# Performance work log

Measured on AMD Instinct MI355X. Metric: run time of the kernel, lower is better.

## Reference

```python
import jax, jax.numpy as jnp
import numpy as np

N, M = 32768, 12          # atoms, neighbors
ORIG, NBR, AF, HF = 92, 41, 64, 128
N_CONV = 3
ATOMS_PER = 32            # atoms per crystal
B = N // ATOMS_PER        # number of crystals
EPS = 1e-5                # BatchNorm eps


def softplus(x):
    return jnp.logaddexp(x, 0.0)


def setup_inputs() -> dict:
    key = jax.random.key(0)
    ks = jax.random.split(key, 24)
    s = 0.05
    return {
        "atom_fea": jax.random.normal(ks[0], (N, ORIG), jnp.float32),
        "nbr_fea": jax.random.normal(ks[1], (N, M, NBR), jnp.float32),
        "nbr_fea_idx": jax.random.randint(ks[2], (N, M), 0, N),
        "crystal_id": jnp.arange(N, dtype=jnp.int32) // ATOMS_PER,
        # embedding: Linear(ORIG -> AF)
        "emb_W": jax.random.normal(ks[3], (ORIG, AF), jnp.float32) * s,
        "emb_b": jnp.zeros((AF,), jnp.float32),
        # per-conv-layer params, stacked over N_CONV
        "conv_W": jax.random.normal(ks[4], (N_CONV, 2 * AF + NBR, 2 * AF), jnp.float32) * s,
        "conv_b": jnp.zeros((N_CONV, 2 * AF), jnp.float32),
        "bn1_g": jnp.ones((N_CONV, 2 * AF), jnp.float32),
        "bn1_b": jnp.zeros((N_CONV, 2 * AF), jnp.float32),
        "bn2_g": jnp.ones((N_CONV, AF), jnp.float32),
        "bn2_b": jnp.zeros((N_CONV, AF), jnp.float32),
        # head: conv_to_fc (AF->HF), fcs[0] (HF->HF), fc_out (HF->1)
        "fc1_W": jax.random.normal(ks[5], (AF, HF), jnp.float32) * s,
        "fc1_b": jnp.zeros((HF,), jnp.float32),
        "fc2_W": jax.random.normal(ks[6], (HF, HF), jnp.float32) * s,
        "fc2_b": jnp.zeros((HF,), jnp.float32),
        "out_W": jax.random.normal(ks[7], (HF, 1), jnp.float32) * s,
        "out_b": jnp.zeros((1,), jnp.float32),
    }


def _batchnorm(x, g, b):
    # training-mode BN over the batch (row) axis, biased variance like torch
    mu = x.mean(axis=0)
    var = x.var(axis=0)
    return (x - mu) * jax.lax.rsqrt(var + EPS) * g + b


def reference(atom_fea, nbr_fea, nbr_fea_idx, crystal_id,
              emb_W, emb_b, conv_W, conv_b, bn1_g, bn1_b, bn2_g, bn2_b,
              fc1_W, fc1_b, fc2_W, fc2_b, out_W, out_b):
    x = atom_fea @ emb_W + emb_b                              # (N, AF)
    for l in range(N_CONV):
        nbr_atom = x[nbr_fea_idx]                             # gather (N, M, AF)
        self_fea = jnp.broadcast_to(x[:, None, :], (N, M, AF))
        tot = jnp.concatenate([self_fea, nbr_atom, nbr_fea], axis=2)  # (N,M,2AF+NBR)
        g = tot @ conv_W[l] + conv_b[l]                       # (N, M, 2AF)
        g = _batchnorm(g.reshape(N * M, 2 * AF), bn1_g[l], bn1_b[l]).reshape(N, M, 2 * AF)
        nbr_filter = jax.nn.sigmoid(g[..., :AF])
        nbr_core = softplus(g[..., AF:])
        summed = jnp.sum(nbr_filter * nbr_core, axis=1)       # (N, AF)
        summed = _batchnorm(summed, bn2_g[l], bn2_b[l])
        x = softplus(x + summed)
    # mean pooling per crystal (equal-size crystals of ATOMS_PER atoms)
    pool = jax.ops.segment_sum(x, crystal_id, num_segments=B) / ATOMS_PER  # (B, AF)
    # seq2: softplus -> conv_to_fc -> dropout(p=0) -> softplus -> Linear -> softplus -> dropout(p=0)
    h = softplus(pool)
    h = softplus(h @ fc1_W + fc1_b)
    h = softplus(h @ fc2_W + fc2_b)
    return h @ out_W + out_b                                  # (B, 1)
```

## Files before the change

kernel.cpp:

```cpp
#include <hip/hip_runtime.h>
#include <cmath>

#define DEV __device__ __forceinline__

constexpr int NA    = 32768;
constexpr int M     = 12;
constexpr int ORIG  = 92;
constexpr int NBR   = 41;
constexpr int AF    = 64;
constexpr int C2    = 128;
constexpr int HF    = 128;
constexpr int NCONV = 3;
constexpr int NM    = NA * M;
constexpr int BB    = 1024;
constexpr int TA    = 4;
constexpr int RT    = TA * M;
constexpr int NTILES = NA / TA;
constexpr int GRID_CONV = 4096;
constexpr int TSTRIDE = GRID_CONV / 2;
constexpr int GRID_APPLY = 2048;
constexpr int WLD2  = 68;
constexpr int ALD   = 44;

DEV float fsig(float x) { return __builtin_amdgcn_rcpf(1.f + __expf(-x)); }
DEV float fsp (float x) { return fmaxf(x, 0.f) + __logf(1.f + __expf(-fabsf(x))); }

DEV void fma4(float4& a, float s, const float4 w) {
    a.x = fmaf(s, w.x, a.x); a.y = fmaf(s, w.y, a.y);
    a.z = fmaf(s, w.z, a.z); a.w = fmaf(s, w.w, a.w);
}
DEV void fma2(float2& a, float s, const float2 w) {
    a.x = fmaf(s, w.x, a.x); a.y = fmaf(s, w.y, a.y);
}
DEV float comp4(const float4 v, int i) { return i == 0 ? v.x : i == 1 ? v.y : i == 2 ? v.z : v.w; }
DEV void add2(float2& a, const float2 b) { a.x += b.x; a.y += b.y; }
DEV void sqa2(float2& a, const float2 b) { a.x = fmaf(b.x, b.x, a.x); a.y = fmaf(b.y, b.y, a.y); }
DEV float2 shxor2(const float2 v, int m) {
    float2 r; r.x = __shfl_xor(v.x, m, 64); r.y = __shfl_xor(v.y, m, 64); return r;
}
DEV void bfly2(float2& v) {
    float2 t = shxor2(v, 16); add2(v, t);
    t = shxor2(v, 32); add2(v, t);
}
DEV unsigned bf16pair(float a, float b) {
    unsigned ua = __float_as_uint(a), ub = __float_as_uint(b);
    ua += 0x7fffu + ((ua >> 16) & 1u);
    ub += 0x7fffu + ((ub >> 16) & 1u);
    return (ua >> 16) | (ub & 0xffff0000u);
}
DEV float2 up2(unsigned u) {
    float2 r;
    r.x = __uint_as_float(u << 16);
    r.y = __uint_as_float(u & 0xffff0000u);
    return r;
}

template<bool FIRST>
__global__ __launch_bounds__(256, 4)
void spx_kernel(const float* __restrict__ xin,
                const float* __restrict__ summed,
                const float* __restrict__ ss2,
                const float* __restrict__ atom_fea,
                const float* __restrict__ embW,
                const float* __restrict__ embb,
                const float* __restrict__ W,
                const float* __restrict__ bias,
                float* __restrict__ xout,
                float* __restrict__ S,
                unsigned* __restrict__ Pb)
{
    __shared__ float xs[16][AF];
    __shared__ float af[FIRST ? 16 * ORIG : 4];

    const int a0 = blockIdx.x * 16, tid = threadIdx.x;

    if (FIRST) {
        for (int i = tid; i < 16 * ORIG; i += 256) af[i] = atom_fea[(size_t)a0 * ORIG + i];
        __syncthreads();
        const int row = tid >> 4, c4 = (tid & 15) * 4;
        float4 acc = *(const float4*)(embb + c4);
        #pragma unroll 4
        for (int k = 0; k < ORIG; ++k)
            fma4(acc, af[row * ORIG + k], *(const float4*)(embW + k * AF + c4));
        *(float4*)&xs[row][c4] = acc;
        *(float4*)(xout + (size_t)(a0 + row) * AF + c4) = acc;
    } else {
        const int row = tid >> 4, c4 = (tid & 15) * 4;
        const size_t o = (size_t)(a0 + row) * AF + c4;
        const float4 xi = *(const float4*)(xin + o);
        const float4 sm = *(const float4*)(summed + o);
        const float4 sc = *(const float4*)(ss2 + c4);
        const float4 sh = *(const float4*)(ss2 + AF + c4);
        float4 ov;
        ov.x = fsp(xi.x + fmaf(sm.x, sc.x, sh.x));
        ov.y = fsp(xi.y + fmaf(sm.y, sc.y, sh.y));
        ov.z = fsp(xi.z + fmaf(sm.z, sc.z, sh.z));
        ov.w = fsp(xi.w + fmaf(sm.w, sc.w, sh.w));
        *(float4*)&xs[row][c4] = ov;
        *(float4*)(xout + o) = ov;
    }
    __syncthreads();

    const int cid = tid & 31, rid = tid >> 5;
    const int c0 = cid * 8, r0 = rid * 2;
    const bool isS = (c0 < 128);
    const int cc = c0 & 127;
    const float* Wb = W + (isS ? 0 : AF * C2) + cc;
    float4 a00, a01, a10, a11;
    if (isS) { a00 = *(const float4*)(bias + cc); a01 = *(const float4*)(bias + cc + 4); }
    else     { a00 = {0,0,0,0}; a01 = {0,0,0,0}; }
    a10 = a00; a11 = a01;
    for (int k = 0; k < AF; ++k) {
        const float4 w0 = *(const float4*)(Wb + k * C2);
        const float4 w1 = *(const float4*)(Wb + k * C2 + 4);
        const float x0 = xs[r0][k], x1 = xs[r0 + 1][k];
        fma4(a00, x0, w0); fma4(a01, x0, w1);
        fma4(a10, x1, w0); fma4(a11, x1, w1);
    }
    if (isS) {
        *(float4*)(S + (size_t)(a0 + r0) * C2 + cc)     = a00;
        *(float4*)(S + (size_t)(a0 + r0) * C2 + cc + 4) = a01;
        *(float4*)(S + (size_t)(a0 + r0 + 1) * C2 + cc)     = a10;
        *(float4*)(S + (size_t)(a0 + r0 + 1) * C2 + cc + 4) = a11;
    } else {
        uint4 u0, u1;
        u0.x = bf16pair(a00.x, a00.y); u0.y = bf16pair(a00.z, a00.w);
        u0.z = bf16pair(a01.x, a01.y); u0.w = bf16pair(a01.z, a01.w);
        u1.x = bf16pair(a10.x, a10.y); u1.y = bf16pair(a10.z, a10.w);
        u1.z = bf16pair(a11.x, a11.y); u1.w = bf16pair(a11.z, a11.w);
        *(uint4*)(Pb + (size_t)(a0 + r0) * 64 + cc / 2)     = u0;
        *(uint4*)(Pb + (size_t)(a0 + r0 + 1) * 64 + cc / 2) = u1;
    }
}

__global__ __launch_bounds__(256, 4)
void conv8_kernel(const float* __restrict__ nbr_fea,
                  const int* __restrict__ idx,
                  const float* __restrict__ W2,
                  const float* __restrict__ S,
                  const unsigned* __restrict__ Pb,
                  float* __restrict__ P1s, float* __restrict__ P1q,
                  unsigned* __restrict__ gout)
{
    __shared__ float W2h[NBR * WLD2];
    __shared__ float sA[RT * ALD];

    const int tid  = threadIdx.x;
    const int cid  = tid & 15;
    const int rid  = tid >> 4;
    const int ch   = blockIdx.x & 1;
    const int c2   = cid * 2;
    const int gf   = ch * 32 + c2;
    const int gc   = 64 + gf;
    const int r0   = rid * 3;
    const int atom = tid >> 6;

    const int q0 = blockIdx.x >> 1;

    int j0, j1, j2;
    float2 svf, svc;
    float st[8];
    {
        const int n0 = q0 * TA;
        const int ib = n0 * M + r0;
        j0 = idx[ib]; j1 = idx[ib + 1]; j2 = idx[ib + 2];
        svf = *(const float2*)(S + (size_t)(n0 + atom) * C2 + gf);
        svc = *(const float2*)(S + (size_t)(n0 + atom) * C2 + gc);
        const float* src = nbr_fea + (size_t)n0 * M * NBR;
        #pragma unroll
        for (int i = 0; i < 8; ++i)
            if (tid + 256 * i < RT * NBR) st[i] = src[tid + 256 * i];
    }

    for (int i = tid; i < NBR * 16; i += 256) {
        const int k = i >> 4, q = i & 15;
        const int srcc = (q < 8) ? (ch * 32 + q * 4) : (64 + ch * 32 + (q - 8) * 4);
        *(float4*)&W2h[k * WLD2 + q * 4] = *(const float4*)(W2 + k * C2 + srcc);
    }

    int soff[8];
    #pragma unroll
    for (int i = 0; i < 8; ++i) {
        const int e = tid + 256 * i;
        if (e < RT * NBR) {
            const int r = (int)(((unsigned)e * 102301u) >> 22);
            soff[i] = r * ALD + (e - r * NBR);
        } else soff[i] = -1;
    }

    float2 sum_f = {0,0}, sum_c = {0,0}, sq_f = {0,0}, sq_c = {0,0};

    for (int it = 0; it < 4; ++it) {
        const int t  = q0 + it * TSTRIDE;
        const int n0 = t * TA;

        const unsigned u0f = Pb[(size_t)j0 * 64 + ch * 16 + cid];
        const unsigned u0c = Pb[(size_t)j0 * 64 + 32 + ch * 16 + cid];
        const unsigned u1f = Pb[(size_t)j1 * 64 + ch * 16 + cid];
        const unsigned u1c = Pb[(size_t)j1 * 64 + 32 + ch * 16 + cid];
        const unsigned u2f = Pb[(size_t)j2 * 64 + ch * 16 + cid];
        const unsigned u2c = Pb[(size_t)j2 * 64 + 32 + ch * 16 + cid];

        const float2 cf = svf, cc = svc;

        __syncthreads();
        #pragma unroll
        for (int i = 0; i < 8; ++i) if (soff[i] >= 0) sA[soff[i]] = st[i];
        __syncthreads();

        if (it < 3) {
            const int nn0 = (t + TSTRIDE) * TA;
            const int ib = nn0 * M + r0;
            j0 = idx[ib]; j1 = idx[ib + 1]; j2 = idx[ib + 2];
            svf = *(const float2*)(S + (size_t)(nn0 + atom) * C2 + gf);
            svc = *(const float2*)(S + (size_t)(nn0 + atom) * C2 + gc);
            const float* src = nbr_fea + (size_t)nn0 * M * NBR;
            #pragma unroll
            for (int i = 0; i < 8; ++i)
                if (tid + 256 * i < RT * NBR) st[i] = src[tid + 256 * i];
        }

        float2 ef0 = {0,0}, ec0 = {0,0}, ef1 = {0,0}, ec1 = {0,0}, ef2 = {0,0}, ec2 = {0,0};
        const float4* A0 = (const float4*)(sA + (r0 + 0) * ALD);
        const float4* A1 = (const float4*)(sA + (r0 + 1) * ALD);
        const float4* A2 = (const float4*)(sA + (r0 + 2) * ALD);
        #pragma unroll 2
        for (int k4 = 0; k4 < 10; ++k4) {
            const float4 a0 = A0[k4], a1 = A1[k4], a2 = A2[k4];
            #pragma unroll
            for (int kk = 0; kk < 4; ++kk) {
                const int k = 4 * k4 + kk;
                const float2 wf = *(const float2*)(W2h + k * WLD2 + c2);
                const float2 wc = *(const float2*)(W2h + k * WLD2 + 32 + c2);
                fma2(ef0, comp4(a0, kk), wf); fma2(ec0, comp4(a0, kk), wc);
                fma2(ef1, comp4(a1, kk), wf); fma2(ec1, comp4(a1, kk), wc);
                fma2(ef2, comp4(a2, kk), wf); fma2(ec2, comp4(a2, kk), wc);
            }
        }
        {
            const float2 wf = *(const float2*)(W2h + 40 * WLD2 + c2);
            const float2 wc = *(const float2*)(W2h + 40 * WLD2 + 32 + c2);
            const float a0s = sA[(r0 + 0) * ALD + 40];
            const float a1s = sA[(r0 + 1) * ALD + 40];
            const float a2s = sA[(r0 + 2) * ALD + 40];
            fma2(ef0, a0s, wf); fma2(ec0, a0s, wc);
            fma2(ef1, a1s, wf); fma2(ec1, a1s, wc);
            fma2(ef2, a2s, wf); fma2(ec2, a2s, wc);
        }

        add2(ef0, cf); add2(ef0, up2(u0f));
        add2(ec0, cc); add2(ec0, up2(u0c));
        add2(ef1, cf); add2(ef1, up2(u1f));
        add2(ec1, cc); add2(ec1, up2(u1c));
        add2(ef2, cf); add2(ef2, up2(u2f));
        add2(ec2, cc); add2(ec2, up2(u2c));

        {
            const size_t row0 = (size_t)(n0 * M + r0) * 64 + ch * 16 + cid;
            gout[row0]       = bf16pair(ef0.x, ef0.y);
            gout[row0 + 32]  = bf16pair(ec0.x, ec0.y);
            gout[row0 + 64]  = bf16pair(ef1.x, ef1.y);
            gout[row0 + 96]  = bf16pair(ec1.x, ec1.y);
            gout[row0 + 128] = bf16pair(ef2.x, ef2.y);
            gout[row0 + 160] = bf16pair(ec2.x, ec2.y);
        }

        add2(sum_f, ef0); add2(sum_f, ef1); add2(sum_f, ef2);
        add2(sum_c, ec0); add2(sum_c, ec1); add2(sum_c, ec2);
        sqa2(sq_f, ef0);  sqa2(sq_f, ef1);  sqa2(sq_f, ef2);
        sqa2(sq_c, ec0);  sqa2(sq_c, ec1);  sqa2(sq_c, ec2);
    }

    bfly2(sum_f); bfly2(sum_c); bfly2(sq_f); bfly2(sq_c);
    __syncthreads();
    if ((tid & 48) == 0) {
        *(float2*)&sA[atom * 64 + c2]            = sum_f;
        *(float2*)&sA[atom * 64 + 32 + c2]       = sum_c;
        *(float2*)&sA[256 + atom * 64 + c2]      = sq_f;
        *(float2*)&sA[256 + atom * 64 + 32 + c2] = sq_c;
    }
    __syncthreads();
    if (tid < 64) {
        P1s[(size_t)blockIdx.x * 64 + tid] = sA[tid] + sA[64 + tid] + sA[128 + tid] + sA[192 + tid];
        P1q[(size_t)blockIdx.x * 64 + tid] = sA[256 + tid] + sA[256 + 64 + tid]
                                           + sA[256 + 128 + tid] + sA[256 + 192 + tid];
    }
}

__global__ __launch_bounds__(256)
void apply_g_kernel(const unsigned* __restrict__ g,
                    const float* __restrict__ ss1,
                    float* __restrict__ summed,
                    float* __restrict__ P2s, float* __restrict__ P2q)
{
    const int tid = threadIdx.x;
    const int al  = tid >> 5;
    const int c2  = tid & 31;
    const int cA  = 2 * c2;
    const float2 scf = *(const float2*)(ss1 + cA);
    const float2 scc = *(const float2*)(ss1 + 64 + cA);
    const float2 shf = *(const float2*)(ss1 + C2 + cA);
    const float2 shc = *(const float2*)(ss1 + C2 + 64 + cA);
    float2 ts = {0.f, 0.f}, tq = {0.f, 0.f};

    for (int grp = blockIdx.x; grp < NA / 8; grp += gridDim.x) {
        const int a = grp * 8 + al;
        const unsigned* gr = g + (size_t)a * M * 64 + c2;
        float2 acc = {0.f, 0.f};
        #pragma unroll
        for (int m = 0; m < M; ++m) {
            const unsigned uf = gr[m * 64];
            const unsigned us = gr[m * 64 + 32];
            const float2 f = up2(uf);
            const float2 s = up2(us);
            acc.x = fmaf(fsig(fmaf(f.x, scf.x, shf.x)), fsp(fmaf(s.x, scc.x, shc.x)), acc.x);
            acc.y = fmaf(fsig(fmaf(f.y, scf.y, shf.y)), fsp(fmaf(s.y, scc.y, shc.y)), acc.y);
        }
        *(float2*)(summed + (size_t)a * AF + cA) = acc;
        ts.x += acc.x; ts.y += acc.y;
        tq.x = fmaf(acc.x, acc.x, tq.x); tq.y = fmaf(acc.y, acc.y, tq.y);
    }

    __shared__ float2 rs[8][32], rq[8][32];
    rs[al][c2] = ts; rq[al][c2] = tq;
    __syncthreads();
    if (tid < 32) {
        float2 s = rs[0][tid], q = rq[0][tid];
        #pragma unroll
        for (int a = 1; a < 8; ++a) {
            s.x += rs[a][tid].x; s.y += rs[a][tid].y;
            q.x += rq[a][tid].x; q.y += rq[a][tid].y;
        }
        *(float2*)(P2s + (size_t)blockIdx.x * AF + 2 * tid) = s;
        *(float2*)(P2q + (size_t)blockIdx.x * AF + 2 * tid) = q;
    }
}

__global__ __launch_bounds__(256)
void bn_finalize_half(const float* __restrict__ Ps, const float* __restrict__ Pq,
                      int rowlen, float invn,
                      const float* __restrict__ gamma, const float* __restrict__ beta,
                      float* __restrict__ ss, int Ctot)
{
    __shared__ float sd[256];
    const int c = blockIdx.x, tid = threadIdx.x;
    const int ch = (c >> 5) & 1;
    const int lc = (c & 31) + ((c >= 64) ? 32 : 0);
    float s = 0.f;
    for (int i = tid; i < TSTRIDE; i += 256) s += Ps[(size_t)(ch + 2 * i) * rowlen + lc];
    sd[tid] = s; __syncthreads();
    for (int st = 128; st > 0; st >>= 1) { if (tid < st) sd[tid] += sd[tid + st]; __syncthreads(); }
    const float total = sd[0];
    __syncthreads();
    float q = 0.f;
    for (int i = tid; i < TSTRIDE; i += 256) q += Pq[(size_t)(ch + 2 * i) * rowlen + lc];
    sd[tid] = q; __syncthreads();
    for (int st = 128; st > 0; st >>= 1) { if (tid < st) sd[tid] += sd[tid + st]; __syncthreads(); }
    if (tid == 0) {
        const float mean = total * invn;
        const float var  = sd[0] * invn - mean * mean;
        const float scl  = gamma[c] * rsqrtf(var + 1e-5f);
        ss[c]        = scl;
        ss[Ctot + c] = beta[c] - mean * scl;
    }
}

__global__ __launch_bounds__(256)
void bn_finalize_plain(const float* __restrict__ Ps, const float* __restrict__ Pq,
                       int npart, int C, float invn,
                       const float* __restrict__ gamma, const float* __restrict__ beta,
                       float* __restrict__ ss)
{
    __shared__ float sd[256];
    const int c = blockIdx.x, tid = threadIdx.x;
    float s = 0.f;
    for (int j = tid; j < npart; j += 256) s += Ps[(size_t)j * C + c];
    sd[tid] = s; __syncthreads();
    for (int st = 128; st > 0; st >>= 1) { if (tid < st) sd[tid] += sd[tid + st]; __syncthreads(); }
    const float total = sd[0];
    __syncthreads();
    float q = 0.f;
    for (int j = tid; j < npart; j += 256) q += Pq[(size_t)j * C + c];
    sd[tid] = q; __syncthreads();
    for (int st = 128; st > 0; st >>= 1) { if (tid < st) sd[tid] += sd[tid + st]; __syncthreads(); }
    if (tid == 0) {
        const float mean = total * invn;
        const float var  = sd[0] * invn - mean * mean;
        const float scl  = gamma[c] * rsqrtf(var + 1e-5f);
        ss[c]     = scl;
        ss[C + c] = beta[c] - mean * scl;
    }
}

__global__ __launch_bounds__(128)
void head_kernel(const float* __restrict__ x,
                 const float* __restrict__ summed,
                 const float* __restrict__ ss2,
                 const float* __restrict__ fc1W, const float* __restrict__ fc1b,
                 const float* __restrict__ fc2W, const float* __restrict__ fc2b,
                 const float* __restrict__ outW, const float* __restrict__ outb,
                 float* __restrict__ out)
{
    __shared__ float l0[AF], l1[HF], rr[2], hs[2][AF];
    const int b = blockIdx.x, tid = threadIdx.x;
    const int col = tid & 63, half = tid >> 6;
    {
        const float sc = ss2[col], sh = ss2[AF + col];
        float s = 0.f;
        #pragma unroll 4
        for (int a = half * 16; a < half * 16 + 16; ++a) {
            const size_t o = (size_t)(b * 32 + a) * AF + col;
            s += fsp(x[o] + fmaf(summed[o], sc, sh));
        }
        hs[half][col] = s;
    }
    __syncthreads();
    if (tid < AF) l0[tid] = fsp((hs[0][tid] + hs[1][tid]) * (1.f / 32.f));
    __syncthreads();
    float acc = fc1b[tid];
    #pragma unroll 4
    for (int k = 0; k < AF; ++k) acc = fmaf(l0[k], fc1W[k * HF + tid], acc);
    l1[tid] = fsp(acc);
    __syncthreads();
    acc = fc2b[tid];
    #pragma unroll 4
    for (int k = 0; k < HF; ++k) acc = fmaf(l1[k], fc2W[k * HF + tid], acc);
    float v = fsp(acc) * outW[tid];
    #pragma unroll
    for (int off = 32; off > 0; off >>= 1) v += __shfl_down(v, off, 64);
    if ((tid & 63) == 0) rr[tid >> 6] = v;
    __syncthreads();
    if (tid == 0) out[b] = rr[0] + rr[1] + outb[0];
}

extern "C" void kernel_launch(void* const* d_in, const int* in_sizes, int n_in,
                              void* d_out, int out_size, void* d_ws, size_t ws_size,
                              hipStream_t stream)
{
    const float* atom_fea = (const float*)d_in[0];
    const float* nbr_fea  = (const float*)d_in[1];
    const int*   nbr_idx  = (const int*)d_in[2];
    const float* emb_W  = (const float*)d_in[4];
    const float* emb_b  = (const float*)d_in[5];
    const float* conv_W = (const float*)d_in[6];
    const float* conv_b = (const float*)d_in[7];
    const float* bn1_g  = (const float*)d_in[8];
    const float* bn1_b  = (const float*)d_in[9];
    const float* bn2_g  = (const float*)d_in[10];
    const float* bn2_b  = (const float*)d_in[11];
    const float* fc1W   = (const float*)d_in[12];
    const float* fc1b   = (const float*)d_in[13];
    const float* fc2W   = (const float*)d_in[14];
    const float* fc2b   = (const float*)d_in[15];
    const float* outW   = (const float*)d_in[16];
    const float* outb   = (const float*)d_in[17];
    float* out = (float*)d_out;
    float* ws  = (float*)d_ws;

    float*    x_a    = ws;
    float*    x_b    = x_a + (size_t)NA * AF;
    float*    Sbuf   = x_b + (size_t)NA * AF;
    unsigned* Pb     = (unsigned*)(Sbuf + (size_t)NA * C2);
    float*    summed = (float*)(Pb + (size_t)NA * 64);
    float*    P1s    = summed + (size_t)NA * AF;
    float*    P1q    = P1s + (size_t)GRID_CONV * 64;
    float*    P2s    = P1q + (size_t)GRID_CONV * 64;
    float*    P2q    = P2s + (size_t)GRID_APPLY * AF;
    float*    ss1    = P2q + (size_t)GRID_APPLY * AF;
    float*    ss2    = ss1 + 2 * C2;
    unsigned* gbuf   = (unsigned*)(ss2 + 2 * AF);

    float* xcur = x_a;
    spx_kernel<true><<<NA / 16, 256, 0, stream>>>(nullptr, nullptr, nullptr,
                                                  atom_fea, emb_W, emb_b,
                                                  conv_W, conv_b, xcur, Sbuf, Pb);
    for (int l = 0; l < NCONV; ++l) {
        const float* W2 = conv_W + (size_t)l * (C2 + NBR) * C2 + (size_t)C2 * C2;
        conv8_kernel<<<GRID_CONV, 256, 0, stream>>>(nbr_fea, nbr_idx, W2,
                                                    Sbuf, Pb, P1s, P1q, gbuf);
        bn_finalize_half<<<C2, 256, 0, stream>>>(P1s, P1q, 64, 1.f / (float)NM,
                                                 bn1_g + l * C2, bn1_b + l * C2, ss1, C2);
        apply_g_kernel<<<GRID_APPLY, 256, 0, stream>>>(gbuf, ss1, summed, P2s, P2q);
        bn_finalize_plain<<<AF, 256, 0, stream>>>(P2s, P2q, GRID_APPLY, AF, 1.f / (float)NA,
                                                  bn2_g + l * AF, bn2_b + l * AF, ss2);
        if (l < NCONV - 1) {
            float* xnext = (xcur == x_a) ? x_b : x_a;
            spx_kernel<false><<<NA / 16, 256, 0, stream>>>(xcur, summed, ss2,
                                                           nullptr, nullptr, nullptr,
                                                           conv_W + (size_t)(l + 1) * (C2 + NBR) * C2,
                                                           conv_b + (size_t)(l + 1) * C2,
                                                           xnext, Sbuf, Pb);
            xcur = xnext;
        }
    }
    head_kernel<<<BB, 128, 0, stream>>>(xcur, summed, ss2,
                                        fc1W, fc1b, fc2W, fc2b, outW, outb, out);
}
```

Baseline: 641.7 us.

## Have each conv block cover all 128 channels with six rows per thread

```diff
diff --git a/kernel.cpp b/kernel.cpp
--- a/kernel.cpp
+++ b/kernel.cpp
@@ -16,10 +16,9 @@
 constexpr int TA    = 4;
 constexpr int RT    = TA * M;
 constexpr int NTILES = NA / TA;
-constexpr int GRID_CONV = 4096;
-constexpr int TSTRIDE = GRID_CONV / 2;
+constexpr int GRID_CONV = 2048;
 constexpr int GRID_APPLY = 2048;
-constexpr int WLD2  = 68;
+constexpr int WLD   = 132;
 constexpr int ALD   = 44;
 
 DEV float fsig(float x) { return __builtin_amdgcn_rcpf(1.f + __expf(-x)); }
@@ -37,10 +36,6 @@
 DEV void sqa2(float2& a, const float2 b) { a.x = fmaf(b.x, b.x, a.x); a.y = fmaf(b.y, b.y, a.y); }
 DEV float2 shxor2(const float2 v, int m) {
     float2 r; r.x = __shfl_xor(v.x, m, 64); r.y = __shfl_xor(v.y, m, 64); return r;
-}
-DEV void bfly2(float2& v) {
-    float2 t = shxor2(v, 16); add2(v, t);
-    t = shxor2(v, 32); add2(v, t);
 }
 DEV unsigned bf16pair(float a, float b) {
     unsigned ua = __float_as_uint(a), ub = __float_as_uint(b);
@@ -142,148 +137,162 @@
                   float* __restrict__ P1s, float* __restrict__ P1q,
                   unsigned* __restrict__ gout)
 {
-    __shared__ float W2h[NBR * WLD2];
+    __shared__ float W2h[NBR * WLD];
     __shared__ float sA[RT * ALD];
 
     const int tid  = threadIdx.x;
-    const int cid  = tid & 15;
-    const int rid  = tid >> 4;
-    const int ch   = blockIdx.x & 1;
+    const int cid  = tid & 31;
+    const int rid  = tid >> 5;
     const int c2   = cid * 2;
-    const int gf   = ch * 32 + c2;
-    const int gc   = 64 + gf;
-    const int r0   = rid * 3;
-    const int atom = tid >> 6;
-
-    const int q0 = blockIdx.x >> 1;
-
-    int j0, j1, j2;
+    const int r0   = rid * 6;
+    const int atom = rid >> 1;
+
+    const int q0 = blockIdx.x;
+
+    int j[6];
     float2 svf, svc;
     float st[8];
     {
         const int n0 = q0 * TA;
         const int ib = n0 * M + r0;
-        j0 = idx[ib]; j1 = idx[ib + 1]; j2 = idx[ib + 2];
-        svf = *(const float2*)(S + (size_t)(n0 + atom) * C2 + gf);
-        svc = *(const float2*)(S + (size_t)(n0 + atom) * C2 + gc);
+        #pragma unroll
+        for (int e = 0; e < 6; ++e) j[e] = idx[ib + e];
+        svf = *(const float2*)(S + (size_t)(n0 + atom) * C2 + c2);
+        svc = *(const float2*)(S + (size_t)(n0 + atom) * C2 + 64 + c2);
         const float* src = nbr_fea + (size_t)n0 * M * NBR;
         #pragma unroll
         for (int i = 0; i < 8; ++i)
-            if (tid + 256 * i < RT * NBR) st[i] = src[tid + 256 * i];
-    }
-
-    for (int i = tid; i < NBR * 16; i += 256) {
-        const int k = i >> 4, q = i & 15;
-        const int srcc = (q < 8) ? (ch * 32 + q * 4) : (64 + ch * 32 + (q - 8) * 4);
-        *(float4*)&W2h[k * WLD2 + q * 4] = *(const float4*)(W2 + k * C2 + srcc);
-    }
-
-    int soff[8];
-    #pragma unroll
-    for (int i = 0; i < 8; ++i) {
-        const int e = tid + 256 * i;
-        if (e < RT * NBR) {
-            const int r = (int)(((unsigned)e * 102301u) >> 22);
-            soff[i] = r * ALD + (e - r * NBR);
-        } else soff[i] = -1;
+            if (i < 7 || tid + 256 * i < RT * NBR) st[i] = src[tid + 256 * i];
+    }
+
+    for (int i = tid; i < NBR * 32; i += 256) {
+        const int k = i >> 5, q = i & 31;
+        *(float4*)&W2h[k * WLD + q * 4] = *(const float4*)(W2 + k * C2 + q * 4);
     }
 
     float2 sum_f = {0,0}, sum_c = {0,0}, sq_f = {0,0}, sq_c = {0,0};
 
     for (int it = 0; it < 4; ++it) {
-        const int t  = q0 + it * TSTRIDE;
+        const int t  = q0 + it * GRID_CONV;
         const int n0 = t * TA;
 
-        const unsigned u0f = Pb[(size_t)j0 * 64 + ch * 16 + cid];
-        const unsigned u0c = Pb[(size_t)j0 * 64 + 32 + ch * 16 + cid];
-        const unsigned u1f = Pb[(size_t)j1 * 64 + ch * 16 + cid];
-        const unsigned u1c = Pb[(size_t)j1 * 64 + 32 + ch * 16 + cid];
-        const unsigned u2f = Pb[(size_t)j2 * 64 + ch * 16 + cid];
-        const unsigned u2c = Pb[(size_t)j2 * 64 + 32 + ch * 16 + cid];
-
+        unsigned uf[6], uc[6];
+        #pragma unroll
+        for (int e = 0; e < 6; ++e) {
+            uf[e] = Pb[(size_t)j[e] * 64 + cid];
+            uc[e] = Pb[(size_t)j[e] * 64 + 32 + cid];
+        }
         const float2 cf = svf, cc = svc;
 
         __syncthreads();
         #pragma unroll
-        for (int i = 0; i < 8; ++i) if (soff[i] >= 0) sA[soff[i]] = st[i];
+        for (int i = 0; i < 8; ++i) {
+            const int e = tid + 256 * i;
+            if (i < 7 || e < RT * NBR) {
+                const int r = (int)(((unsigned)e * 102301u) >> 22);
+                sA[r * ALD + (e - r * NBR)] = st[i];
+            }
+        }
         __syncthreads();
 
         if (it < 3) {
-            const int nn0 = (t + TSTRIDE) * TA;
+            const int nn0 = (t + GRID_CONV) * TA;
             const int ib = nn0 * M + r0;
-            j0 = idx[ib]; j1 = idx[ib + 1]; j2 = idx[ib + 2];
-            svf = *(const float2*)(S + (size_t)(nn0 + atom) * C2 + gf);
-            svc = *(const float2*)(S + (size_t)(nn0 + atom) * C2 + gc);
+            #pragma unroll
+            for (int e = 0; e < 6; ++e) j[e] = idx[ib + e];
+            svf = *(const float2*)(S + (size_t)(nn0 + atom) * C2 + c2);
+            svc = *(const float2*)(S + (size_t)(nn0 + atom) * C2 + 64 + c2);
             const float* src = nbr_fea + (size_t)nn0 * M * NBR;
             #pragma unroll
             for (int i = 0; i < 8; ++i)
-                if (tid + 256 * i < RT * NBR) st[i] = src[tid + 256 * i];
-        }
-
-        float2 ef0 = {0,0}, ec0 = {0,0}, ef1 = {0,0}, ec1 = {0,0}, ef2 = {0,0}, ec2 = {0,0};
-        const float4* A0 = (const float4*)(sA + (r0 + 0) * ALD);
-        const float4* A1 = (const float4*)(sA + (r0 + 1) * ALD);
-        const float4* A2 = (const float4*)(sA + (r0 + 2) * ALD);
+                if (i < 7 || tid + 256 * i < RT * NBR) st[i] = src[tid + 256 * i];
+        }
+
+        float2 ef0 = {0,0}, ef1 = {0,0}, ef2 = {0,0}, ef3 = {0,0}, ef4 = {0,0}, ef5 = {0,0};
+        float2 ec0 = {0,0}, ec1 = {0,0}, ec2 = {0,0}, ec3 = {0,0}, ec4 = {0,0}, ec5 = {0,0};
+        const float* Ab = sA + r0 * ALD;
         #pragma unroll 2
         for (int k4 = 0; k4 < 10; ++k4) {
-            const float4 a0 = A0[k4], a1 = A1[k4], a2 = A2[k4];
+            const float4 a0 = *(const float4*)(Ab + 0 * ALD + k4 * 4);
+            const float4 a1 = *(const float4*)(Ab + 1 * ALD + k4 * 4);
+            const float4 a2 = *(const float4*)(Ab + 2 * ALD + k4 * 4);
+            const float4 a3 = *(const float4*)(Ab + 3 * ALD + k4 * 4);
+            const float4 a4 = *(const float4*)(Ab + 4 * ALD + k4 * 4);
+            const float4 a5 = *(const float4*)(Ab + 5 * ALD + k4 * 4);
             #pragma unroll
             for (int kk = 0; kk < 4; ++kk) {
                 const int k = 4 * k4 + kk;
-                const float2 wf = *(const float2*)(W2h + k * WLD2 + c2);
-                const float2 wc = *(const float2*)(W2h + k * WLD2 + 32 + c2);
+                const float2 wf = *(const float2*)(W2h + k * WLD + c2);
+                const float2 wc = *(const float2*)(W2h + k * WLD + 64 + c2);
                 fma2(ef0, comp4(a0, kk), wf); fma2(ec0, comp4(a0, kk), wc);
                 fma2(ef1, comp4(a1, kk), wf); fma2(ec1, comp4(a1, kk), wc);
                 fma2(ef2, comp4(a2, kk), wf); fma2(ec2, comp4(a2, kk), wc);
+                fma2(ef3, comp4(a3, kk), wf); fma2(ec3, comp4(a3, kk), wc);
+                fma2(ef4, comp4(a4, kk), wf); fma2(ec4, comp4(a4, kk), wc);
+                fma2(ef5, comp4(a5, kk), wf); fma2(ec5, comp4(a5, kk), wc);
             }
         }
         {
-            const float2 wf = *(const float2*)(W2h + 40 * WLD2 + c2);
-            const float2 wc = *(const float2*)(W2h + 40 * WLD2 + 32 + c2);
-            const float a0s = sA[(r0 + 0) * ALD + 40];
-            const float a1s = sA[(r0 + 1) * ALD + 40];
-            const float a2s = sA[(r0 + 2) * ALD + 40];
-            fma2(ef0, a0s, wf); fma2(ec0, a0s, wc);
-            fma2(ef1, a1s, wf); fma2(ec1, a1s, wc);
-            fma2(ef2, a2s, wf); fma2(ec2, a2s, wc);
-        }
-
-        add2(ef0, cf); add2(ef0, up2(u0f));
-        add2(ec0, cc); add2(ec0, up2(u0c));
-        add2(ef1, cf); add2(ef1, up2(u1f));
-        add2(ec1, cc); add2(ec1, up2(u1c));
-        add2(ef2, cf); add2(ef2, up2(u2f));
-        add2(ec2, cc); add2(ec2, up2(u2c));
-
+            const float2 wf = *(const float2*)(W2h + 40 * WLD + c2);
+            const float2 wc = *(const float2*)(W2h + 40 * WLD + 64 + c2);
+            const float b0 = Ab[0 * ALD + 40], b1 = Ab[1 * ALD + 40], b2 = Ab[2 * ALD + 40];
+            const float b3 = Ab[3 * ALD + 40], b4 = Ab[4 * ALD + 40], b5 = Ab[5 * ALD + 40];
+            fma2(ef0, b0, wf); fma2(ec0, b0, wc);
+            fma2(ef1, b1, wf); fma2(ec1, b1, wc);
+            fma2(ef2, b2, wf); fma2(ec2, b2, wc);
+            fma2(ef3, b3, wf); fma2(ec3, b3, wc);
+            fma2(ef4, b4, wf); fma2(ec4, b4, wc);
+            fma2(ef5, b5, wf); fma2(ec5, b5, wc);
+        }
+
+        const size_t row0 = (size_t)(n0 * M + r0) * 64 + cid;
         {
-            const size_t row0 = (size_t)(n0 * M + r0) * 64 + ch * 16 + cid;
-            gout[row0]       = bf16pair(ef0.x, ef0.y);
-            gout[row0 + 32]  = bf16pair(ec0.x, ec0.y);
-            gout[row0 + 64]  = bf16pair(ef1.x, ef1.y);
-            gout[row0 + 96]  = bf16pair(ec1.x, ec1.y);
-            gout[row0 + 128] = bf16pair(ef2.x, ef2.y);
-            gout[row0 + 160] = bf16pair(ec2.x, ec2.y);
-        }
-
-        add2(sum_f, ef0); add2(sum_f, ef1); add2(sum_f, ef2);
-        add2(sum_c, ec0); add2(sum_c, ec1); add2(sum_c, ec2);
-        sqa2(sq_f, ef0);  sqa2(sq_f, ef1);  sqa2(sq_f, ef2);
-        sqa2(sq_c, ec0);  sqa2(sq_c, ec1);  sqa2(sq_c, ec2);
-    }
-
-    bfly2(sum_f); bfly2(sum_c); bfly2(sq_f); bfly2(sq_c);
-    __syncthreads();
-    if ((tid & 48) == 0) {
-        *(float2*)&sA[atom * 64 + c2]            = sum_f;
-        *(float2*)&sA[atom * 64 + 32 + c2]       = sum_c;
-        *(float2*)&sA[256 + atom * 64 + c2]      = sq_f;
-        *(float2*)&sA[256 + atom * 64 + 32 + c2] = sq_c;
-    }
-    __syncthreads();
-    if (tid < 64) {
-        P1s[(size_t)blockIdx.x * 64 + tid] = sA[tid] + sA[64 + tid] + sA[128 + tid] + sA[192 + tid];
-        P1q[(size_t)blockIdx.x * 64 + tid] = sA[256 + tid] + sA[256 + 64 + tid]
-                                           + sA[256 + 128 + tid] + sA[256 + 192 + tid];
+            add2(ef0, cf); add2(ef0, up2(uf[0])); add2(ec0, cc); add2(ec0, up2(uc[0]));
+            add2(ef1, cf); add2(ef1, up2(uf[1])); add2(ec1, cc); add2(ec1, up2(uc[1]));
+            add2(ef2, cf); add2(ef2, up2(uf[2])); add2(ec2, cc); add2(ec2, up2(uc[2]));
+            add2(ef3, cf); add2(ef3, up2(uf[3])); add2(ec3, cc); add2(ec3, up2(uc[3]));
+            add2(ef4, cf); add2(ef4, up2(uf[4])); add2(ec4, cc); add2(ec4, up2(uc[4]));
+            add2(ef5, cf); add2(ef5, up2(uf[5])); add2(ec5, cc); add2(ec5, up2(uc[5]));
+            gout[row0 + 0 * 64]      = bf16pair(ef0.x, ef0.y);
+            gout[row0 + 0 * 64 + 32] = bf16pair(ec0.x, ec0.y);
+            gout[row0 + 1 * 64]      = bf16pair(ef1.x, ef1.y);
+            gout[row0 + 1 * 64 + 32] = bf16pair(ec1.x, ec1.y);
+            gout[row0 + 2 * 64]      = bf16pair(ef2.x, ef2.y);
+            gout[row0 + 2 * 64 + 32] = bf16pair(ec2.x, ec2.y);
+            gout[row0 + 3 * 64]      = bf16pair(ef3.x, ef3.y);
+            gout[row0 + 3 * 64 + 32] = bf16pair(ec3.x, ec3.y);
+            gout[row0 + 4 * 64]      = bf16pair(ef4.x, ef4.y);
+            gout[row0 + 4 * 64 + 32] = bf16pair(ec4.x, ec4.y);
+            gout[row0 + 5 * 64]      = bf16pair(ef5.x, ef5.y);
+            gout[row0 + 5 * 64 + 32] = bf16pair(ec5.x, ec5.y);
+            add2(sum_f, ef0); add2(sum_f, ef1); add2(sum_f, ef2);
+            add2(sum_f, ef3); add2(sum_f, ef4); add2(sum_f, ef5);
+            add2(sum_c, ec0); add2(sum_c, ec1); add2(sum_c, ec2);
+            add2(sum_c, ec3); add2(sum_c, ec4); add2(sum_c, ec5);
+            sqa2(sq_f, ef0); sqa2(sq_f, ef1); sqa2(sq_f, ef2);
+            sqa2(sq_f, ef3); sqa2(sq_f, ef4); sqa2(sq_f, ef5);
+            sqa2(sq_c, ec0); sqa2(sq_c, ec1); sqa2(sq_c, ec2);
+            sqa2(sq_c, ec3); sqa2(sq_c, ec4); sqa2(sq_c, ec5);
+        }
+    }
+
+    { float2 t2 = shxor2(sum_f, 32); add2(sum_f, t2); }
+    { float2 t2 = shxor2(sum_c, 32); add2(sum_c, t2); }
+    { float2 t2 = shxor2(sq_f, 32);  add2(sq_f, t2);  }
+    { float2 t2 = shxor2(sq_c, 32);  add2(sq_c, t2);  }
+    __syncthreads();
+    const int w = tid >> 6;
+    if ((tid & 32) == 0) {
+        *(float2*)&sA[w * 128 + c2]            = sum_f;
+        *(float2*)&sA[w * 128 + 64 + c2]       = sum_c;
+        *(float2*)&sA[512 + w * 128 + c2]      = sq_f;
+        *(float2*)&sA[512 + w * 128 + 64 + c2] = sq_c;
+    }
+    __syncthreads();
+    if (tid < 128) {
+        P1s[(size_t)blockIdx.x * C2 + tid] = sA[tid] + sA[128 + tid] + sA[256 + tid] + sA[384 + tid];
+        P1q[(size_t)blockIdx.x * C2 + tid] = sA[512 + tid] + sA[512 + 128 + tid]
+                                           + sA[512 + 256 + tid] + sA[512 + 384 + tid];
     }
 }
 
@@ -333,35 +342,6 @@
         }
         *(float2*)(P2s + (size_t)blockIdx.x * AF + 2 * tid) = s;
         *(float2*)(P2q + (size_t)blockIdx.x * AF + 2 * tid) = q;
-    }
-}
-
-__global__ __launch_bounds__(256)
-void bn_finalize_half(const float* __restrict__ Ps, const float* __restrict__ Pq,
-                      int rowlen, float invn,
-                      const float* __restrict__ gamma, const float* __restrict__ beta,
-                      float* __restrict__ ss, int Ctot)
-{
-    __shared__ float sd[256];
-    const int c = blockIdx.x, tid = threadIdx.x;
-    const int ch = (c >> 5) & 1;
-    const int lc = (c & 31) + ((c >= 64) ? 32 : 0);
-    float s = 0.f;
-    for (int i = tid; i < TSTRIDE; i += 256) s += Ps[(size_t)(ch + 2 * i) * rowlen + lc];
-    sd[tid] = s; __syncthreads();
-    for (int st = 128; st > 0; st >>= 1) { if (tid < st) sd[tid] += sd[tid + st]; __syncthreads(); }
-    const float total = sd[0];
-    __syncthreads();
-    float q = 0.f;
-    for (int i = tid; i < TSTRIDE; i += 256) q += Pq[(size_t)(ch + 2 * i) * rowlen + lc];
-    sd[tid] = q; __syncthreads();
-    for (int st = 128; st > 0; st >>= 1) { if (tid < st) sd[tid] += sd[tid + st]; __syncthreads(); }
-    if (tid == 0) {
-        const float mean = total * invn;
-        const float var  = sd[0] * invn - mean * mean;
-        const float scl  = gamma[c] * rsqrtf(var + 1e-5f);
-        ss[c]        = scl;
-        ss[Ctot + c] = beta[c] - mean * scl;
     }
 }
 
@@ -463,8 +443,8 @@
     unsigned* Pb     = (unsigned*)(Sbuf + (size_t)NA * C2);
     float*    summed = (float*)(Pb + (size_t)NA * 64);
     float*    P1s    = summed + (size_t)NA * AF;
-    float*    P1q    = P1s + (size_t)GRID_CONV * 64;
-    float*    P2s    = P1q + (size_t)GRID_CONV * 64;
+    float*    P1q    = P1s + (size_t)GRID_CONV * C2;
+    float*    P2s    = P1q + (size_t)GRID_CONV * C2;
     float*    P2q    = P2s + (size_t)GRID_APPLY * AF;
     float*    ss1    = P2q + (size_t)GRID_APPLY * AF;
     float*    ss2    = ss1 + 2 * C2;
@@ -478,8 +458,8 @@
         const float* W2 = conv_W + (size_t)l * (C2 + NBR) * C2 + (size_t)C2 * C2;
         conv8_kernel<<<GRID_CONV, 256, 0, stream>>>(nbr_fea, nbr_idx, W2,
                                                     Sbuf, Pb, P1s, P1q, gbuf);
-        bn_finalize_half<<<C2, 256, 0, stream>>>(P1s, P1q, 64, 1.f / (float)NM,
-                                                 bn1_g + l * C2, bn1_b + l * C2, ss1, C2);
+        bn_finalize_plain<<<C2, 256, 0, stream>>>(P1s, P1q, GRID_CONV, C2, 1.f / (float)NM,
+                                                  bn1_g + l * C2, bn1_b + l * C2, ss1);
         apply_g_kernel<<<GRID_APPLY, 256, 0, stream>>>(gbuf, ss1, summed, P2s, P2q);
         bn_finalize_plain<<<AF, 256, 0, stream>>>(P2s, P2q, GRID_APPLY, AF, 1.f / (float)NA,
                                                   bn2_g + l * AF, bn2_b + l * AF, ss2);
```

New measurement: 646.9 us. About the same (+0.8%).
